# Kernel optimization log

Hardware: AMD Instinct MI355X
Metric: run time of the kernel (lower is better)

Reference implementation:

```python
import jax, jax.numpy as jnp
import numpy as np
from jax import lax
from jax.scipy.special import logsumexp

B, L, D = 64, 256, 512
NUM_CLASS, NREF, NNEG = 10, 50, 100
BLUR = 0.05
EPS_FINAL = BLUR ** 2  # geomloss: eps = blur**p with p=2
MARGIN = 10.0

# epsilon-scaling schedule (geomloss anneals eps geometrically, scaling=0.5),
# then extra iterations at the final eps for convergence.
_sched = []
_e = 8.0
while _e > EPS_FINAL:
    _sched.append(_e)
    _e *= 0.5
_sched += [EPS_FINAL] * 15
EPS_SCHED = jnp.asarray(np.array(_sched, np.float32))


def _cost(x, y):
    # geomloss p=2 cost: |x - y|^2 / 2   -> [N, M]
    return 0.5 * (jnp.sum(x * x, -1)[:, None] + jnp.sum(y * y, -1)[None, :] - 2.0 * (x @ y.T))


def _ot(a, x, b, y):
    """Entropic OT value <a,f>+<b,g> via log-domain Sinkhorn with eps-scaling.
    a,b are (possibly zero-padded) weights; x,y point clouds."""
    C = _cost(x, y)
    loga = jnp.where(a > 0, jnp.log(jnp.maximum(a, 1e-30)), -1e9)
    logb = jnp.where(b > 0, jnp.log(jnp.maximum(b, 1e-30)), -1e9)

    def body(fg, eps):
        f, g = fg
        f = -eps * logsumexp(logb[None, :] + (g[None, :] - C) / eps, axis=1)
        g = -eps * logsumexp(loga[:, None] + (f[:, None] - C) / eps, axis=0)
        return (f, g), None

    (f, g), _ = lax.scan(body, (jnp.zeros_like(a), jnp.zeros_like(b)), EPS_SCHED)
    return jnp.sum(a * f) + jnp.sum(b * g)


def _forward(anchor, weight, anchor_out_neg, t0, grade, grade_neg):
    Cn = t0.shape[0]
    w_ref = jnp.full((t0.shape[1],), 1.0 / t0.shape[1], anchor.dtype)
    w_neg = jnp.full((anchor_out_neg.shape[1],), 1.0 / anchor_out_neg.shape[1], anchor.dtype)

    # cross OT anchor_i vs every class reference cloud: [B, C]
    ot_cross = jax.vmap(lambda a, x: jax.vmap(lambda y: _ot(a, x, w_ref, y))(t0))(weight, anchor)
    # self terms for debiasing
    ot_aa = jax.vmap(lambda a, x: _ot(a, x, a, x))(weight, anchor)            # [B]
    ot_tt = jax.vmap(lambda y: _ot(w_ref, y, w_ref, y))(t0)                    # [C]
    ot_nn = jax.vmap(lambda y: _ot(w_neg, y, w_neg, y))(anchor_out_neg)        # [B]

    # debiased Sinkhorn divergence S = OT_ab - 0.5 OT_aa - 0.5 OT_bb
    S = ot_cross - 0.5 * ot_aa[:, None] - 0.5 * ot_tt[None, :]                 # [B, C]
    pos = jnp.take_along_axis(S, grade[:, None], axis=1)[:, 0]                 # [B]

    # after the torch k-loop, k == num_class-1 (loop-variable leak) -> t0[last]
    t_last = t0[Cn - 1]
    ot_ln = jax.vmap(lambda y: _ot(w_ref, t_last, w_neg, y))(anchor_out_neg)   # [B]
    S_last = ot_ln - 0.5 * ot_tt[Cn - 1] - 0.5 * ot_nn

    t_g = t0[grade_neg]                                                        # [B, NREF, D]
    ot_gn = jax.vmap(lambda yt, yn: _ot(w_ref, yt, w_neg, yn))(t_g, anchor_out_neg)
    S_gn = ot_gn - 0.5 * ot_tt[grade_neg] - 0.5 * ot_nn

    # hinge over all classes k != grade[i], plus the neg-cloud entry (index -1)
    notself = jnp.arange(Cn)[None, :] != grade[:, None]
    hinge_cls = jnp.sum(jnp.where(notself, jax.nn.relu(pos[:, None] - S + MARGIN), 0.0), axis=1)
    hinge_neg = jax.nn.relu(pos - S_last + MARGIN)
    loss_dif = jnp.abs(S_gn - S_last)
    return jnp.mean(hinge_cls + hinge_neg + loss_dif)


def setup_inputs() -> dict:
    key = jax.random.key(0)
    ks = jax.random.split(key, 7)
    anchor = jax.random.normal(ks[0], (B, L, D), jnp.float32)
    length_anchor = jax.random.randint(ks[1], (B,), L // 2, L + 1)
    grade = jax.random.randint(ks[2], (B,), 0, NUM_CLASS)
    w = jax.random.uniform(ks[3], (B, L), jnp.float32, 1e-3, 1.0)
    mask = jnp.arange(L)[None, :] < length_anchor[:, None]
    w = w * mask
    weight = w / jnp.sum(w, axis=1, keepdims=True)  # normalized histogram per sample
    anchor_out_neg = jax.random.normal(ks[4], (B, NNEG, D), jnp.float32)
    grade_neg = jax.random.randint(ks[5], (B,), 0, NUM_CLASS)
    t0 = jax.random.normal(ks[6], (NUM_CLASS, NREF, D), jnp.float32)
    return {"anchor": anchor, "length_anchor": length_anchor, "grade": grade,
            "weight": weight, "anchor_out_neg": anchor_out_neg,
            "grade_neg": grade_neg, "t0": t0, "num_class": NUM_CLASS}


def reference(anchor, length_anchor, grade, weight, anchor_out_neg, grade_neg, t0, num_class):
    # length_anchor is encoded in the zero-padding of `weight` (masked positions
    # have weight 0 and drop out of the OT); num_class == t0.shape[0].
    return _forward(anchor, weight, anchor_out_neg, t0, grade, grade_neg)
```

## Files before the change

kernel.cpp:

```cpp
#include <hip/hip_runtime.h>

#define NB   64
#define LA   256
#define DD   512
#define NCLS 10
#define NREF 50
#define NNEG 100
#define MARGIN 10.0f
#define NITER 27

#define LOG2E 1.44269504f
#define LN2   0.69314718f
#define LC50  (-3.9120230054f)
#define LC100 (-4.6051701860f)

#define OFF_CX   ((size_t)0)
#define SZ_CX    ((size_t)64*500*256)
#define OFF_CAA  (OFF_CX + SZ_CX)
#define SZ_CAA   ((size_t)64*256*256)
#define OFF_CNN  (OFF_CAA + SZ_CAA)
#define SZ_CNN   ((size_t)64*100*100)
#define OFF_CLN  (OFF_CNN + SZ_CNN)
#define SZ_CLN   ((size_t)64*50*100)
#define OFF_CGN  (OFF_CLN + SZ_CLN)
#define SZ_CGN   ((size_t)64*50*100)
#define OFF_CTT  (OFF_CGN + SZ_CGN)
#define SZ_CTT   ((size_t)10*50*50)
#define OFF_SQA  (OFF_CTT + SZ_CTT)
#define OFF_SQN  (OFF_SQA + (size_t)64*256)
#define OFF_SQT  (OFF_SQN + (size_t)64*100)
#define OFF_OTX  (OFF_SQT + (size_t)500)
#define OFF_OTAA (OFF_OTX + (size_t)640)
#define OFF_OTNN (OFF_OTAA + (size_t)64)
#define OFF_OTLN (OFF_OTNN + (size_t)64)
#define OFF_OTGN (OFF_OTLN + (size_t)64)
#define OFF_OTTT (OFF_OTGN + (size_t)64)

__device__ __forceinline__ float eps_at(int it) {
    return (it < 12) ? ldexpf(8.0f, -it) : 0.0025f;
}

__device__ __forceinline__ float block_sum256(float v, float* red, int tid) {
    #pragma unroll
    for (int off = 1; off < 64; off <<= 1) v += __shfl_xor(v, off);
    if ((tid & 63) == 0) red[tid >> 6] = v;
    __syncthreads();
    return red[0] + red[1] + red[2] + red[3];
}

__global__ __launch_bounds__(256) void sq_kernel(const float* __restrict__ anchor,
                                                 const float* __restrict__ neg,
                                                 const float* __restrict__ t0,
                                                 float* __restrict__ ws) {
    int gw   = (blockIdx.x * 256 + threadIdx.x) >> 6;
    int lane = threadIdx.x & 63;
    const int nA = NB * LA, nN = NB * NNEG, nT = NCLS * NREF;
    if (gw >= nA + nN + nT) return;
    const float* row; float* outp;
    if (gw < nA)           { row = anchor + (size_t)gw * DD;          outp = ws + OFF_SQA + gw; }
    else if (gw < nA + nN) { int r = gw - nA;      row = neg + (size_t)r * DD; outp = ws + OFF_SQN + r; }
    else                   { int r = gw - nA - nN; row = t0  + (size_t)r * DD; outp = ws + OFF_SQT + r; }
    const float4* r4 = (const float4*)row;
    float4 u = r4[lane * 2], v = r4[lane * 2 + 1];
    float s = u.x*u.x + u.y*u.y + u.z*u.z + u.w*u.w
            + v.x*v.x + v.y*v.y + v.z*v.z + v.w*v.w;
    #pragma unroll
    for (int off = 1; off < 64; off <<= 1) s += __shfl_xor(s, off);
    if (lane == 0) *outp = 0.5f * s;
}

#define CTM 128
#define CTK 16
__global__ __launch_bounds__(256) void cost128(const float* __restrict__ anchor,
                                               const float* __restrict__ neg,
                                               const float* __restrict__ t0,
                                               const int* __restrict__ gneg,
                                               float* __restrict__ ws) {
    __shared__ __align__(16) float As[CTK][CTM];
    __shared__ __align__(16) float Bs[CTK][CTM];
    int bid = blockIdx.x, tid = threadIdx.x;
    const float *X, *Y, *sqx, *sqy;
    float* Cout; int N, M, ldc, r0, c0;
    bool tr = false;
    if (bid < 512) {
        int b = bid >> 3, t = bid & 7;
        r0 = (t >> 2) * 128; c0 = (t & 3) * 128;
        X = anchor + (size_t)b * LA * DD; Y = t0; N = LA; M = 500; ldc = 500;
        Cout = ws + OFF_CX + (size_t)b * 500 * 256;
        sqx = ws + OFF_SQA + b * LA; sqy = ws + OFF_SQT;
        tr = true;
    } else if (bid < 768) {
        int b2 = bid - 512; int b = b2 >> 2, t = b2 & 3;
        r0 = (t >> 1) * 128; c0 = (t & 1) * 128;
        X = Y = anchor + (size_t)b * LA * DD; N = M = LA; ldc = LA;
        Cout = ws + OFF_CAA + (size_t)b * LA * LA;
        sqx = sqy = ws + OFF_SQA + b * LA;
    } else if (bid < 832) {
        int b = bid - 768; r0 = 0; c0 = 0;
        X = Y = neg + (size_t)b * NNEG * DD; N = M = NNEG; ldc = NNEG;
        Cout = ws + OFF_CNN + (size_t)b * NNEG * NNEG;
        sqx = sqy = ws + OFF_SQN + b * NNEG;
    } else if (bid < 896) {
        int b = bid - 832; r0 = 0; c0 = 0;
        X = t0 + (size_t)9 * NREF * DD; Y = neg + (size_t)b * NNEG * DD;
        N = NREF; M = NNEG; ldc = NNEG;
        Cout = ws + OFF_CLN + (size_t)b * NREF * NNEG;
        sqx = ws + OFF_SQT + 9 * NREF; sqy = ws + OFF_SQN + b * NNEG;
    } else if (bid < 960) {
        int b = bid - 896; r0 = 0; c0 = 0;
        int gc = gneg[b];
        X = t0 + (size_t)gc * NREF * DD; Y = neg + (size_t)b * NNEG * DD;
        N = NREF; M = NNEG; ldc = NNEG;
        Cout = ws + OFF_CGN + (size_t)b * NREF * NNEG;
        sqx = ws + OFF_SQT + gc * NREF; sqy = ws + OFF_SQN + b * NNEG;
    } else {
        int c = bid - 960; r0 = 0; c0 = 0;
        X = Y = t0 + (size_t)c * NREF * DD; N = M = NREF; ldc = NREF;
        Cout = ws + OFF_CTT + (size_t)c * NREF * NREF;
        sqx = sqy = ws + OFF_SQT + c * NREF;
    }
    int row = tid & 127, kq = tid >> 7;
    int tx = tid & 15, ty = tid >> 4;
    bool xok = (r0 + row) < N, yok = (c0 + row) < M;
    const float* xrow = X + (size_t)(r0 + row) * DD + kq * 8;
    const float* yrow = Y + (size_t)(c0 + row) * DD + kq * 8;
    float acc[8][8];
    #pragma unroll
    for (int a = 0; a < 8; a++)
        #pragma unroll
        for (int b = 0; b < 8; b++) acc[a][b] = 0.f;
    for (int k0 = 0; k0 < DD; k0 += CTK) {
        float4 xa0 = xok ? *(const float4*)(xrow + k0)     : make_float4(0,0,0,0);
        float4 xa1 = xok ? *(const float4*)(xrow + k0 + 4) : make_float4(0,0,0,0);
        float4 ya0 = yok ? *(const float4*)(yrow + k0)     : make_float4(0,0,0,0);
        float4 ya1 = yok ? *(const float4*)(yrow + k0 + 4) : make_float4(0,0,0,0);
        __syncthreads();
        int kb = kq * 8;
        As[kb+0][row]=xa0.x; As[kb+1][row]=xa0.y; As[kb+2][row]=xa0.z; As[kb+3][row]=xa0.w;
        As[kb+4][row]=xa1.x; As[kb+5][row]=xa1.y; As[kb+6][row]=xa1.z; As[kb+7][row]=xa1.w;
        Bs[kb+0][row]=ya0.x; Bs[kb+1][row]=ya0.y; Bs[kb+2][row]=ya0.z; Bs[kb+3][row]=ya0.w;
        Bs[kb+4][row]=ya1.x; Bs[kb+5][row]=ya1.y; Bs[kb+6][row]=ya1.z; Bs[kb+7][row]=ya1.w;
        __syncthreads();
        #pragma unroll
        for (int k = 0; k < CTK; k++) {
            float4 a0 = *(const float4*)&As[k][ty << 3];
            float4 a1 = *(const float4*)&As[k][(ty << 3) + 4];
            float4 b0 = *(const float4*)&Bs[k][tx << 3];
            float4 b1 = *(const float4*)&Bs[k][(tx << 3) + 4];
            float av[8] = {a0.x,a0.y,a0.z,a0.w,a1.x,a1.y,a1.z,a1.w};
            float bv[8] = {b0.x,b0.y,b0.z,b0.w,b1.x,b1.y,b1.z,b1.w};
            #pragma unroll
            for (int a = 0; a < 8; a++)
                #pragma unroll
                for (int b = 0; b < 8; b++)
                    acc[a][b] = fmaf(av[a], bv[b], acc[a][b]);
        }
    }
    #pragma unroll
    for (int a = 0; a < 8; a++) {
        int n = r0 + (ty << 3) + a;
        if (n < N) {
            float sx = sqx[n];
            #pragma unroll
            for (int b = 0; b < 8; b++) {
                int m = c0 + (tx << 3) + b;
                if (m < M) {
                    float v = sx + sqy[m] - acc[a][b];
                    if (tr) Cout[(size_t)m * 256 + n] = v;
                    else    Cout[(size_t)n * ldc + m] = v;
                }
            }
        }
    }
}

__global__ __launch_bounds__(1024, 1) void aa_sink_reg(const float* __restrict__ weight,
                                                       float* __restrict__ ws) {
    __shared__ __align__(16) float ahS[256];
    __shared__ float pm[4][256];
    __shared__ float ps[4][256];
    __shared__ float red[16];
    int i = blockIdx.x, tid = threadIdx.x;
    int w = tid >> 6, lane = tid & 63;
    int q = w >> 2;
    int c = ((w & 3) << 6) | lane;
    const float* Cg = ws + OFF_CAA + ((size_t)i << 16);
    float Creg[64];
    #pragma unroll
    for (int k = 0; k < 64; ++k)
        Creg[k] = Cg[(size_t)((q << 6) + k) * 256 + c];
    float wgt = weight[(size_t)i * LA + c];
    float la = (wgt > 0.f) ? __logf(fmaxf(wgt, 1e-30f)) : -1e9f;
    float h = 0.f, fs = 0.f;
    if (q == 0) ahS[c] = 8.0f * la;
    __syncthreads();
    int r4 = q << 4;
    const float4* ah4 = (const float4*)ahS;
    for (int app = 0; app < 54; ++app) {
        float eps = eps_at(app >> 1);
        float m0 = -3.4e38f, m1 = -3.4e38f, m2 = -3.4e38f, m3 = -3.4e38f;
        #pragma unroll
        for (int k = 0; k < 16; ++k) {
            float4 av = ah4[r4 + k];
            m0 = fmaxf(m0, av.x - Creg[4*k+0]);
            m1 = fmaxf(m1, av.y - Creg[4*k+1]);
            m2 = fmaxf(m2, av.z - Creg[4*k+2]);
            m3 = fmaxf(m3, av.w - Creg[4*k+3]);
        }
        pm[q][c] = fmaxf(fmaxf(m0, m1), fmaxf(m2, m3));
        __syncthreads();
        float m = fmaxf(fmaxf(pm[0][c], pm[1][c]), fmaxf(pm[2][c], pm[3][c]));
        float ie2 = (1.0f / eps) * LOG2E;
        float s0 = 0.f, s1 = 0.f, s2 = 0.f, s3 = 0.f;
        #pragma unroll
        for (int k = 0; k < 16; ++k) {
            float4 av = ah4[r4 + k];
            s0 += exp2f((av.x - Creg[4*k+0] - m) * ie2);
            s1 += exp2f((av.y - Creg[4*k+1] - m) * ie2);
            s2 += exp2f((av.z - Creg[4*k+2] - m) * ie2);
            s3 += exp2f((av.w - Creg[4*k+3] - m) * ie2);
        }
        ps[q][c] = (s0 + s1) + (s2 + s3);
        __syncthreads();
        float s = (ps[0][c] + ps[1][c]) + (ps[2][c] + ps[3][c]);
        h = -fmaf(eps * LN2, __log2f(s), m);
        if (app == 52) fs = h;
        if (q == 0) {
            float epsn = eps_at((app + 1) >> 1);
            ahS[c] = fmaf(epsn, la, h);
        }
        __syncthreads();
    }
    float contrib = (q == 0) ? wgt * (fs + h) : 0.f;
    #pragma unroll
    for (int off = 1; off < 64; off <<= 1) contrib += __shfl_xor(contrib, off);
    if (lane == 0) red[w] = contrib;
    __syncthreads();
    if (tid == 0) {
        float s = 0.f;
        #pragma unroll
        for (int k = 0; k < 16; ++k) s += red[k];
        ws[OFF_OTAA + i] = s;
    }
}

__global__ __launch_bounds__(256, 3) void sink_rest(const float* __restrict__ weight,
                                                    float* __restrict__ ws) {
    __shared__ __align__(16) float smem[13324];
    float* red = smem + 13320;
    int bid = blockIdx.x, tid = threadIdx.x;

    if (bid < 640) {
        int ii = bid;
        int i = ii / 10, c = ii - i * 10;
        float* CsT = smem;
        float* agS = smem + 13000;
        float* gSp = smem + 13260;
        const float* Cgbase = ws + OFF_CX + (size_t)i * (500 * 256) + (size_t)c * (50 * 256);
        for (int e = tid; e < 3200; e += 256) {
            int r = e >> 6, n4 = (e & 63) << 2;
            *(float4*)&CsT[r * 260 + n4] = *(const float4*)&Cgbase[(size_t)e << 2];
        }
        float w = weight[(size_t)i * LA + tid];
        float la_r = (w > 0.f) ? __logf(fmaxf(w, 1e-30f)) : -1e9f;
        if (tid < 52) gSp[tid] = (tid < 50) ? 0.f : -1.0e30f;
        __syncthreads();
        float Creg[52];
        #pragma unroll
        for (int r = 0; r < 52; ++r) Creg[r] = (r < 50) ? CsT[r * 260 + tid] : 3.0e30f;
        int grp = tid >> 4, j = tid & 15;
        for (int it = 0; it < NITER; ++it) {
            float eps = eps_at(it), ie2 = (1.0f / eps) * LOG2E;
            {
                const float4* g4 = (const float4*)gSp;
                float m0=-3.4e38f, m1=-3.4e38f, m2=-3.4e38f, m3=-3.4e38f;
                #pragma unroll
                for (int k = 0; k < 13; ++k) {
                    float4 gv = g4[k];
                    m0 = fmaxf(m0, gv.x - Creg[4*k+0]);
                    m1 = fmaxf(m1, gv.y - Creg[4*k+1]);
                    m2 = fmaxf(m2, gv.z - Creg[4*k+2]);
                    m3 = fmaxf(m3, gv.w - Creg[4*k+3]);
                }
                float m = fmaxf(fmaxf(m0, m1), fmaxf(m2, m3));
                float s0=0.f, s1=0.f, s2=0.f, s3=0.f;
                #pragma unroll
                for (int k = 0; k < 13; ++k) {
                    float4 gv = g4[k];
                    s0 += exp2f((gv.x - Creg[4*k+0] - m) * ie2);
                    s1 += exp2f((gv.y - Creg[4*k+1] - m) * ie2);
                    s2 += exp2f((gv.z - Creg[4*k+2] - m) * ie2);
                    s3 += exp2f((gv.w - Creg[4*k+3] - m) * ie2);
                }
                float L = fmaf(eps * LN2, __log2f((s0+s1)+(s2+s3)), m);
                float f = -fmaf(eps, LC50, L);
                agS[tid] = fmaf(eps, la_r, f);
            }
            __syncthreads();
            float4 agr[4];
            #pragma unroll
            for (int q = 0; q < 4; ++q)
                agr[q] = *(const float4*)&agS[(j << 2) + (q << 6)];
            for (int o = grp; o < 50; o += 16) {
                const float* Cr = &CsT[o * 260];
                float u[16];
                #pragma unroll
                for (int q = 0; q < 4; ++q) {
                    float4 cv = *(const float4*)&Cr[(j << 2) + (q << 6)];
                    u[4*q+0] = agr[q].x - cv.x;
                    u[4*q+1] = agr[q].y - cv.y;
                    u[4*q+2] = agr[q].z - cv.z;
                    u[4*q+3] = agr[q].w - cv.w;
                }
                float a0 = fmaxf(fmaxf(u[0], u[4]),  fmaxf(u[8],  u[12]));
                float a1 = fmaxf(fmaxf(u[1], u[5]),  fmaxf(u[9],  u[13]));
                float a2 = fmaxf(fmaxf(u[2], u[6]),  fmaxf(u[10], u[14]));
                float a3 = fmaxf(fmaxf(u[3], u[7]),  fmaxf(u[11], u[15]));
                float m = fmaxf(fmaxf(a0, a1), fmaxf(a2, a3));
                #pragma unroll
                for (int off = 1; off < 16; off <<= 1) m = fmaxf(m, __shfl_xor(m, off));
                float s0=0.f, s1=0.f, s2=0.f, s3=0.f;
                #pragma unroll
                for (int k = 0; k < 16; ++k) {
                    float e = exp2f((u[k] - m) * ie2);
                    if ((k & 3) == 0) s0 += e;
                    else if ((k & 3) == 1) s1 += e;
                    else if ((k & 3) == 2) s2 += e;
                    else s3 += e;
                }
                float s = (s0 + s1) + (s2 + s3);
                #pragma unroll
                for (int off = 1; off < 16; off <<= 1) s += __shfl_xor(s, off);
                if (j == 0) gSp[o] = -fmaf(eps * LN2, __log2f(s), m);
            }
            __syncthreads();
        }
        float f_t = agS[tid] - 0.0025f * la_r;
        float contrib = w * f_t + (tid < 50 ? 0.02f * gSp[tid] : 0.f);
        contrib = block_sum256(contrib, red, tid);
        if (tid == 0) ws[OFF_OTX + ii] = contrib;

    } else if (bid < 704) {
        int inst = bid - 640;
        const float* Cg = ws + OFF_CNN + (size_t)inst * 10000;
        float* ahS = smem;
        float* pmS = smem + 104;
        float* psS = smem + 304;
        bool act = tid < 200;
        int q = tid / 100, c = tid - 100 * q;
        float Creg[52];
        if (act) {
            #pragma unroll
            for (int k = 0; k < 52; ++k) {
                int r = q * 52 + k;
                Creg[k] = (r < 100) ? Cg[(size_t)r * 100 + c] : 3.0e30f;
            }
        }
        if (tid < 100) ahS[tid] = 8.0f * LC100;
        if (tid >= 100 && tid < 104) ahS[tid] = -1.0e30f;
        __syncthreads();
        float h = 0.f, fs = 0.f, m = 0.f;
        for (int app = 0; app < 54; ++app) {
            float eps = eps_at(app >> 1);
            if (act) {
                const float4* ah4 = (const float4*)(ahS + q * 52);
                float m0=-3.4e38f, m1=-3.4e38f, m2=-3.4e38f, m3=-3.4e38f;
                #pragma unroll
                for (int k = 0; k < 13; ++k) {
                    float4 av = ah4[k];
                    m0 = fmaxf(m0, av.x - Creg[4*k+0]);
                    m1 = fmaxf(m1, av.y - Creg[4*k+1]);
                    m2 = fmaxf(m2, av.z - Creg[4*k+2]);
                    m3 = fmaxf(m3, av.w - Creg[4*k+3]);
                }
                pmS[q * 100 + c] = fmaxf(fmaxf(m0, m1), fmaxf(m2, m3));
            }
            __syncthreads();
            if (act) {
                m = fmaxf(pmS[c], pmS[100 + c]);
                float ie2 = (1.0f / eps) * LOG2E;
                const float4* ah4 = (const float4*)(ahS + q * 52);
                float s0=0.f, s1=0.f, s2=0.f, s3=0.f;
                #pragma unroll
                for (int k = 0; k < 13; ++k) {
                    float4 av = ah4[k];
                    s0 += exp2f((av.x - Creg[4*k+0] - m) * ie2);
                    s1 += exp2f((av.y - Creg[4*k+1] - m) * ie2);
                    s2 += exp2f((av.z - Creg[4*k+2] - m) * ie2);
                    s3 += exp2f((av.w - Creg[4*k+3] - m) * ie2);
                }
                psS[q * 100 + c] = (s0 + s1) + (s2 + s3);
            }
            __syncthreads();
            if (act) {
                float s = psS[c] + psS[100 + c];
                h = -fmaf(eps * LN2, __log2f(s), m);
                if (app == 52) fs = h;
                if (q == 0) {
                    float epsn = eps_at((app + 1) >> 1);
                    ahS[c] = fmaf(epsn, LC100, h);
                }
            }
            __syncthreads();
        }
        float contrib = (act && q == 0) ? 0.01f * (fs + h) : 0.f;
        contrib = block_sum256(contrib, red, tid);
        if (tid == 0) ws[OFF_OTNN + inst] = contrib;

    } else if (bid < 832) {
        int q2 = bid - 704;
        const float* Cg = (q2 < 64) ? ws + OFF_CLN + (size_t)q2 * 5000
                                    : ws + OFF_CGN + (size_t)(q2 - 64) * 5000;
        float* outp = (q2 < 64) ? ws + OFF_OTLN + q2 : ws + OFF_OTGN + (q2 - 64);
        float* gSp = smem;
        float* fSp = smem + 100;
        float* pmf = smem + 156;
        float* psf = smem + 406;
        float* pmg = smem + 656;
        float* psg = smem + 856;
        bool actf = tid < 250; int rf = tid / 5, c5 = tid - 5 * rf;
        bool actg = tid < 200; int cg = tid >> 1, hg = tid & 1;
        float Cf[20], Cgr[28];
        if (actf) {
            #pragma unroll
            for (int k = 0; k < 20; ++k) Cf[k] = Cg[(size_t)rf * 100 + c5 * 20 + k];
        }
        if (actg) {
            #pragma unroll
            for (int k = 0; k < 28; ++k) {
                int r = hg * 28 + k;
                Cgr[k] = (r < 50) ? Cg[(size_t)r * 100 + cg] : 3.0e30f;
            }
        }
        if (tid < 100) gSp[tid] = 8.0f * LC100;
        if (tid < 6) fSp[50 + tid] = -1.0e30f;
        __syncthreads();
        float fr = 0.f, gr = 0.f, mf = 0.f, mg = 0.f;
        for (int it = 0; it < NITER; ++it) {
            float eps = eps_at(it), ie2 = (1.0f / eps) * LOG2E;
            if (actf) {
                const float4* g4 = (const float4*)(gSp + c5 * 20);
                float m0=-3.4e38f, m1=-3.4e38f, m2=-3.4e38f, m3=-3.4e38f;
                #pragma unroll
                for (int k = 0; k < 5; ++k) {
                    float4 gv = g4[k];
                    m0 = fmaxf(m0, gv.x - Cf[4*k+0]);
                    m1 = fmaxf(m1, gv.y - Cf[4*k+1]);
                    m2 = fmaxf(m2, gv.z - Cf[4*k+2]);
                    m3 = fmaxf(m3, gv.w - Cf[4*k+3]);
                }
                pmf[c5 * 50 + rf] = fmaxf(fmaxf(m0, m1), fmaxf(m2, m3));
            }
            __syncthreads();
            if (actf) {
                mf = fmaxf(fmaxf(pmf[rf], pmf[50 + rf]),
                     fmaxf(fmaxf(pmf[100 + rf], pmf[150 + rf]), pmf[200 + rf]));
                const float4* g4 = (const float4*)(gSp + c5 * 20);
                float s0=0.f, s1=0.f, s2=0.f, s3=0.f;
                #pragma unroll
                for (int k = 0; k < 5; ++k) {
                    float4 gv = g4[k];
                    s0 += exp2f((gv.x - Cf[4*k+0] - mf) * ie2);
                    s1 += exp2f((gv.y - Cf[4*k+1] - mf) * ie2);
                    s2 += exp2f((gv.z - Cf[4*k+2] - mf) * ie2);
                    s3 += exp2f((gv.w - Cf[4*k+3] - mf) * ie2);
                }
                psf[c5 * 50 + rf] = (s0 + s1) + (s2 + s3);
            }
            __syncthreads();
            if (actf) {
                float s = psf[rf] + psf[50 + rf] + psf[100 + rf] + psf[150 + rf] + psf[200 + rf];
                fr = -fmaf(eps * LN2, __log2f(s), mf);
                if (c5 == 0) fSp[rf] = fmaf(eps, LC50, fr);
            }
            __syncthreads();
            if (actg) {
                const float4* f4 = (const float4*)(fSp + hg * 28);
                float m0=-3.4e38f, m1=-3.4e38f, m2=-3.4e38f, m3=-3.4e38f;
                #pragma unroll
                for (int k = 0; k < 7; ++k) {
                    float4 fv = f4[k];
                    m0 = fmaxf(m0, fv.x - Cgr[4*k+0]);
                    m1 = fmaxf(m1, fv.y - Cgr[4*k+1]);
                    m2 = fmaxf(m2, fv.z - Cgr[4*k+2]);
                    m3 = fmaxf(m3, fv.w - Cgr[4*k+3]);
                }
                pmg[hg * 100 + cg] = fmaxf(fmaxf(m0, m1), fmaxf(m2, m3));
            }
            __syncthreads();
            if (actg) {
                mg = fmaxf(pmg[cg], pmg[100 + cg]);
                const float4* f4 = (const float4*)(fSp + hg * 28);
                float s0=0.f, s1=0.f, s2=0.f, s3=0.f;
                #pragma unroll
                for (int k = 0; k < 7; ++k) {
                    float4 fv = f4[k];
                    s0 += exp2f((fv.x - Cgr[4*k+0] - mg) * ie2);
                    s1 += exp2f((fv.y - Cgr[4*k+1] - mg) * ie2);
                    s2 += exp2f((fv.z - Cgr[4*k+2] - mg) * ie2);
                    s3 += exp2f((fv.w - Cgr[4*k+3] - mg) * ie2);
                }
                psg[hg * 100 + cg] = (s0 + s1) + (s2 + s3);
            }
            __syncthreads();
            if (actg) {
                float s = psg[cg] + psg[100 + cg];
                gr = -fmaf(eps * LN2, __log2f(s), mg);
                if (hg == 0) {
                    float epsn = eps_at(it + 1);
                    gSp[cg] = fmaf(epsn, LC100, gr);
                }
            }
            __syncthreads();
        }
        float contrib = 0.f;
        if (actf && c5 == 0) contrib += 0.02f * fr;
        if (actg && hg == 0) contrib += 0.01f * gr;
        contrib = block_sum256(contrib, red, tid);
        if (tid == 0) *outp = contrib;

    } else {
        int inst = bid - 832;
        const float* Cg = ws + OFF_CTT + (size_t)inst * 2500;
        float* ahS = smem;
        bool act = tid < 50;
        float Creg[52];
        if (act) {
            #pragma unroll
            for (int k = 0; k < 52; ++k)
                Creg[k] = (k < 50) ? Cg[(size_t)k * 50 + tid] : 3.0e30f;
        }
        if (tid < 50) ahS[tid] = 8.0f * LC50;
        if (tid >= 50 && tid < 52) ahS[tid] = -1.0e30f;
        __syncthreads();
        float h = 0.f, fs = 0.f;
        const float4* ah4 = (const float4*)ahS;
        for (int app = 0; app < 54; ++app) {
            float eps = eps_at(app >> 1);
            if (act) {
                float m0=-3.4e38f, m1=-3.4e38f, m2=-3.4e38f, m3=-3.4e38f;
                #pragma unroll
                for (int k = 0; k < 13; ++k) {
                    float4 av = ah4[k];
                    m0 = fmaxf(m0, av.x - Creg[4*k+0]);
                    m1 = fmaxf(m1, av.y - Creg[4*k+1]);
                    m2 = fmaxf(m2, av.z - Creg[4*k+2]);
                    m3 = fmaxf(m3, av.w - Creg[4*k+3]);
                }
                float m = fmaxf(fmaxf(m0, m1), fmaxf(m2, m3));
                float ie2 = (1.0f / eps) * LOG2E;
                float s0=0.f, s1=0.f, s2=0.f, s3=0.f;
                #pragma unroll
                for (int k = 0; k < 13; ++k) {
                    float4 av = ah4[k];
                    s0 += exp2f((av.x - Creg[4*k+0] - m) * ie2);
                    s1 += exp2f((av.y - Creg[4*k+1] - m) * ie2);
                    s2 += exp2f((av.z - Creg[4*k+2] - m) * ie2);
                    s3 += exp2f((av.w - Creg[4*k+3] - m) * ie2);
                }
                h = -fmaf(eps * LN2, __log2f((s0+s1)+(s2+s3)), m);
                if (app == 52) fs = h;
            }
            __syncthreads();
            if (act) {
                float epsn = eps_at((app + 1) >> 1);
                ahS[tid] = fmaf(epsn, LC50, h);
            }
            __syncthreads();
        }
        float contrib = act ? 0.02f * (fs + h) : 0.f;
        contrib = block_sum256(contrib, red, tid);
        if (tid == 0) ws[OFF_OTTT + inst] = contrib;
    }
}

__global__ void assemble_kernel(const int* __restrict__ grade, const int* __restrict__ gneg,
                                const float* __restrict__ ws, float* __restrict__ out) {
    int i = threadIdx.x;
    float total = 0.f;
    if (i < 64) {
        float aa  = ws[OFF_OTAA + i];
        float nn  = ws[OFF_OTNN + i];
        float lnv = ws[OFF_OTLN + i];
        float gnv = ws[OFF_OTGN + i];
        int g  = grade[i];
        int gi = gneg[i];
        float tt9 = ws[OFF_OTTT + 9];
        float ttg = ws[OFF_OTTT + gi];
        float Slast = lnv - 0.5f * tt9 - 0.5f * nn;
        float Sgn   = gnv - 0.5f * ttg - 0.5f * nn;
        float Sv[10];
        #pragma unroll
        for (int k = 0; k < 10; k++)
            Sv[k] = ws[OFF_OTX + i * 10 + k] - 0.5f * aa - 0.5f * ws[OFF_OTTT + k];
        float pos = 0.f;
        #pragma unroll
        for (int k = 0; k < 10; k++) pos = (k == g) ? Sv[k] : pos;
        float hc = 0.f;
        #pragma unroll
        for (int k = 0; k < 10; k++)
            if (k != g) hc += fmaxf(pos - Sv[k] + MARGIN, 0.f);
        float hn = fmaxf(pos - Slast + MARGIN, 0.f);
        total = hc + hn + fabsf(Sgn - Slast);
    }
    #pragma unroll
    for (int off = 1; off < 64; off <<= 1) total += __shfl_xor(total, off);
    if (i == 0) out[0] = total * (1.0f / 64.0f);
}

extern "C" void kernel_launch(void* const* d_in, const int* in_sizes, int n_in,
                              void* d_out, int out_size, void* d_ws, size_t ws_size,
                              hipStream_t stream) {
    const float* anchor = (const float*)d_in[0];
    const int*   grade  = (const int*)d_in[2];
    const float* weight = (const float*)d_in[3];
    const float* neg    = (const float*)d_in[4];
    const int*   gneg   = (const int*)d_in[5];
    const float* t0     = (const float*)d_in[6];
    float* ws  = (float*)d_ws;
    float* out = (float*)d_out;

    sq_kernel      <<<5821, 256, 0, stream>>>(anchor, neg, t0, ws);
    cost128        <<<970, 256, 0, stream>>>(anchor, neg, t0, gneg, ws);
    aa_sink_reg    <<<64, 1024, 0, stream>>>(weight, ws);
    sink_rest      <<<842, 256, 0, stream>>>(weight, ws);
    assemble_kernel<<<1, 64, 0, stream>>>(grade, gneg, ws, out);
}
```

Before: 733.2 us.

## Cut barriers in Sinkhorn loops via shuffles and double-buffered potentials

The aa kernel now places the four row-groups of each column inside one wavefront and combines their partial max and sum with cross-lane shuffles instead of shared-memory partials. Potential vectors are double-buffered, so each iteration needs one barrier instead of three. The nn, ln/gn and tt paths of sink_rest likewise stop splitting rows across threads: each active thread keeps a full row or column of C in registers, which also removes the intermediate barriers. This trades parallelism and higher register use (up to 100 floats per thread) in the small blocks for less synchronisation; the ln/gn path also keeps leftover redundant fr computations.

```diff
diff --git a/kernel.cpp b/kernel.cpp
--- a/kernel.cpp
+++ b/kernel.cpp
@@ -176,62 +176,57 @@
 
 __global__ __launch_bounds__(1024, 1) void aa_sink_reg(const float* __restrict__ weight,
                                                        float* __restrict__ ws) {
-    __shared__ __align__(16) float ahS[256];
-    __shared__ float pm[4][256];
-    __shared__ float ps[4][256];
+    __shared__ __align__(16) float ah[2][256];
     __shared__ float red[16];
     int i = blockIdx.x, tid = threadIdx.x;
     int w = tid >> 6, lane = tid & 63;
-    int q = w >> 2;
-    int c = ((w & 3) << 6) | lane;
+    int c = (w << 4) | (lane & 15);
+    int rg = lane >> 4;
     const float* Cg = ws + OFF_CAA + ((size_t)i << 16);
     float Creg[64];
     #pragma unroll
     for (int k = 0; k < 64; ++k)
-        Creg[k] = Cg[(size_t)((q << 6) + k) * 256 + c];
+        Creg[k] = Cg[(size_t)((rg << 6) + k) * 256 + c];
     float wgt = weight[(size_t)i * LA + c];
     float la = (wgt > 0.f) ? __logf(fmaxf(wgt, 1e-30f)) : -1e9f;
     float h = 0.f, fs = 0.f;
-    if (q == 0) ahS[c] = 8.0f * la;
+    if (rg == 0) ah[0][c] = 8.0f * la;
     __syncthreads();
-    int r4 = q << 4;
-    const float4* ah4 = (const float4*)ahS;
     for (int app = 0; app < 54; ++app) {
         float eps = eps_at(app >> 1);
-        float m0 = -3.4e38f, m1 = -3.4e38f, m2 = -3.4e38f, m3 = -3.4e38f;
+        const float4* a4 = (const float4*)(ah[app & 1]) + (rg << 4);
+        float m0=-3.4e38f, m1=-3.4e38f, m2=-3.4e38f, m3=-3.4e38f;
         #pragma unroll
         for (int k = 0; k < 16; ++k) {
-            float4 av = ah4[r4 + k];
+            float4 av = a4[k];
             m0 = fmaxf(m0, av.x - Creg[4*k+0]);
             m1 = fmaxf(m1, av.y - Creg[4*k+1]);
             m2 = fmaxf(m2, av.z - Creg[4*k+2]);
             m3 = fmaxf(m3, av.w - Creg[4*k+3]);
         }
-        pm[q][c] = fmaxf(fmaxf(m0, m1), fmaxf(m2, m3));
-        __syncthreads();
-        float m = fmaxf(fmaxf(pm[0][c], pm[1][c]), fmaxf(pm[2][c], pm[3][c]));
+        float m = fmaxf(fmaxf(m0, m1), fmaxf(m2, m3));
+        m = fmaxf(m, __shfl_xor(m, 16));
+        m = fmaxf(m, __shfl_xor(m, 32));
         float ie2 = (1.0f / eps) * LOG2E;
-        float s0 = 0.f, s1 = 0.f, s2 = 0.f, s3 = 0.f;
+        float s0=0.f, s1=0.f, s2=0.f, s3=0.f;
         #pragma unroll
         for (int k = 0; k < 16; ++k) {
-            float4 av = ah4[r4 + k];
+            float4 av = a4[k];
             s0 += exp2f((av.x - Creg[4*k+0] - m) * ie2);
             s1 += exp2f((av.y - Creg[4*k+1] - m) * ie2);
             s2 += exp2f((av.z - Creg[4*k+2] - m) * ie2);
             s3 += exp2f((av.w - Creg[4*k+3] - m) * ie2);
         }
-        ps[q][c] = (s0 + s1) + (s2 + s3);
-        __syncthreads();
-        float s = (ps[0][c] + ps[1][c]) + (ps[2][c] + ps[3][c]);
+        float s = (s0 + s1) + (s2 + s3);
+        s += __shfl_xor(s, 16);
+        s += __shfl_xor(s, 32);
         h = -fmaf(eps * LN2, __log2f(s), m);
         if (app == 52) fs = h;
-        if (q == 0) {
-            float epsn = eps_at((app + 1) >> 1);
-            ahS[c] = fmaf(epsn, la, h);
-        }
-        __syncthreads();
-    }
-    float contrib = (q == 0) ? wgt * (fs + h) : 0.f;
+        float epsn = eps_at((app + 1) >> 1);
+        if (rg == 0) ah[(app + 1) & 1][c] = fmaf(epsn, la, h);
+        __syncthreads();
+    }
+    float contrib = (rg == 0) ? wgt * (fs + h) : 0.f;
     #pragma unroll
     for (int off = 1; off < 64; off <<= 1) contrib += __shfl_xor(contrib, off);
     if (lane == 0) red[w] = contrib;
@@ -343,67 +338,48 @@
     } else if (bid < 704) {
         int inst = bid - 640;
         const float* Cg = ws + OFF_CNN + (size_t)inst * 10000;
-        float* ahS = smem;
-        float* pmS = smem + 104;
-        float* psS = smem + 304;
-        bool act = tid < 200;
-        int q = tid / 100, c = tid - 100 * q;
-        float Creg[52];
+        float* ahb = smem;
+        bool act = tid < 100;
+        float Creg[100];
         if (act) {
             #pragma unroll
-            for (int k = 0; k < 52; ++k) {
-                int r = q * 52 + k;
-                Creg[k] = (r < 100) ? Cg[(size_t)r * 100 + c] : 3.0e30f;
-            }
-        }
-        if (tid < 100) ahS[tid] = 8.0f * LC100;
-        if (tid >= 100 && tid < 104) ahS[tid] = -1.0e30f;
-        __syncthreads();
-        float h = 0.f, fs = 0.f, m = 0.f;
+            for (int k = 0; k < 100; ++k) Creg[k] = Cg[(size_t)k * 100 + tid];
+        }
+        if (tid < 100) ahb[tid] = 8.0f * LC100;
+        __syncthreads();
+        float h = 0.f, fs = 0.f;
         for (int app = 0; app < 54; ++app) {
             float eps = eps_at(app >> 1);
             if (act) {
-                const float4* ah4 = (const float4*)(ahS + q * 52);
+                const float4* a4 = (const float4*)(ahb + (app & 1) * 100);
                 float m0=-3.4e38f, m1=-3.4e38f, m2=-3.4e38f, m3=-3.4e38f;
                 #pragma unroll
-                for (int k = 0; k < 13; ++k) {
-                    float4 av = ah4[k];
+                for (int k = 0; k < 25; ++k) {
+                    float4 av = a4[k];
                     m0 = fmaxf(m0, av.x - Creg[4*k+0]);
                     m1 = fmaxf(m1, av.y - Creg[4*k+1]);
                     m2 = fmaxf(m2, av.z - Creg[4*k+2]);
                     m3 = fmaxf(m3, av.w - Creg[4*k+3]);
                 }
-                pmS[q * 100 + c] = fmaxf(fmaxf(m0, m1), fmaxf(m2, m3));
-            }
-            __syncthreads();
-            if (act) {
-                m = fmaxf(pmS[c], pmS[100 + c]);
+                float m = fmaxf(fmaxf(m0, m1), fmaxf(m2, m3));
                 float ie2 = (1.0f / eps) * LOG2E;
-                const float4* ah4 = (const float4*)(ahS + q * 52);
                 float s0=0.f, s1=0.f, s2=0.f, s3=0.f;
                 #pragma unroll
-                for (int k = 0; k < 13; ++k) {
-                    float4 av = ah4[k];
+                for (int k = 0; k < 25; ++k) {
+                    float4 av = a4[k];
                     s0 += exp2f((av.x - Creg[4*k+0] - m) * ie2);
                     s1 += exp2f((av.y - Creg[4*k+1] - m) * ie2);
                     s2 += exp2f((av.z - Creg[4*k+2] - m) * ie2);
                     s3 += exp2f((av.w - Creg[4*k+3] - m) * ie2);
                 }
-                psS[q * 100 + c] = (s0 + s1) + (s2 + s3);
+                h = -fmaf(eps * LN2, __log2f((s0+s1)+(s2+s3)), m);
+                if (app == 52) fs = h;
+                float epsn = eps_at((app + 1) >> 1);
+                ahb[((app + 1) & 1) * 100 + tid] = fmaf(epsn, LC100, h);
             }
             __syncthreads();
-            if (act) {
-                float s = psS[c] + psS[100 + c];
-                h = -fmaf(eps * LN2, __log2f(s), m);
-                if (app == 52) fs = h;
-                if (q == 0) {
-                    float epsn = eps_at((app + 1) >> 1);
-                    ahS[c] = fmaf(epsn, LC100, h);
-                }
-            }
-            __syncthreads();
-        }
-        float contrib = (act && q == 0) ? 0.01f * (fs + h) : 0.f;
+        }
+        float contrib = act ? 0.01f * (fs + h) : 0.f;
         contrib = block_sum256(contrib, red, tid);
         if (tid == 0) ws[OFF_OTNN + inst] = contrib;
 
@@ -412,117 +388,92 @@
         const float* Cg = (q2 < 64) ? ws + OFF_CLN + (size_t)q2 * 5000
                                     : ws + OFF_CGN + (size_t)(q2 - 64) * 5000;
         float* outp = (q2 < 64) ? ws + OFF_OTLN + q2 : ws + OFF_OTGN + (q2 - 64);
-        float* gSp = smem;
-        float* fSp = smem + 100;
-        float* pmf = smem + 156;
-        float* psf = smem + 406;
-        float* pmg = smem + 656;
-        float* psg = smem + 856;
-        bool actf = tid < 250; int rf = tid / 5, c5 = tid - 5 * rf;
-        bool actg = tid < 200; int cg = tid >> 1, hg = tid & 1;
-        float Cf[20], Cgr[28];
+        float* gS = smem;
+        float* fS = smem + 104;
+        bool actf = tid < 50;
+        bool actg = (tid >= 64) && (tid < 164);
+        int cg = tid - 64;
+        float Creg[100];
         if (actf) {
             #pragma unroll
-            for (int k = 0; k < 20; ++k) Cf[k] = Cg[(size_t)rf * 100 + c5 * 20 + k];
-        }
-        if (actg) {
-            #pragma unroll
-            for (int k = 0; k < 28; ++k) {
-                int r = hg * 28 + k;
-                Cgr[k] = (r < 50) ? Cg[(size_t)r * 100 + cg] : 3.0e30f;
-            }
-        }
-        if (tid < 100) gSp[tid] = 8.0f * LC100;
-        if (tid < 6) fSp[50 + tid] = -1.0e30f;
-        __syncthreads();
-        float fr = 0.f, gr = 0.f, mf = 0.f, mg = 0.f;
+            for (int k = 0; k < 100; ++k) Creg[k] = Cg[(size_t)tid * 100 + k];
+        } else if (actg) {
+            #pragma unroll
+            for (int k = 0; k < 52; ++k)
+                Creg[k] = (k < 50) ? Cg[(size_t)k * 100 + cg] : 3.0e30f;
+        }
+        if (tid < 100) gS[tid] = 8.0f * LC100;
+        if (tid == 0) { fS[50] = -1.0e30f; fS[51] = -1.0e30f; }
+        __syncthreads();
+        float fr = 0.f, gr = 0.f;
         for (int it = 0; it < NITER; ++it) {
             float eps = eps_at(it), ie2 = (1.0f / eps) * LOG2E;
             if (actf) {
-                const float4* g4 = (const float4*)(gSp + c5 * 20);
+                const float4* g4 = (const float4*)gS;
                 float m0=-3.4e38f, m1=-3.4e38f, m2=-3.4e38f, m3=-3.4e38f;
                 #pragma unroll
-                for (int k = 0; k < 5; ++k) {
+                for (int k = 0; k < 25; ++k) {
                     float4 gv = g4[k];
-                    m0 = fmaxf(m0, gv.x - Cf[4*k+0]);
-                    m1 = fmaxf(m1, gv.y - Cf[4*k+1]);
-                    m2 = fmaxf(m2, gv.z - Cf[4*k+2]);
-                    m3 = fmaxf(m3, gv.w - Cf[4*k+3]);
-                }
-                pmf[c5 * 50 + rf] = fmaxf(fmaxf(m0, m1), fmaxf(m2, m3));
-            }
-            __syncthreads();
-            if (actf) {
-                mf = fmaxf(fmaxf(pmf[rf], pmf[50 + rf]),
-                     fmaxf(fmaxf(pmf[100 + rf], pmf[150 + rf]), pmf[200 + rf]));
-                const float4* g4 = (const float4*)(gSp + c5 * 20);
+                    m0 = fmaxf(m0, gv.x - Creg[4*k+0]);
+                    m1 = fmaxf(m1, gv.y - Creg[4*k+1]);
+                    m2 = fmaxf(m2, gv.z - Creg[4*k+2]);
+                    m3 = fmaxf(m3, gv.w - Creg[4*k+3]);
+                }
+                float m = fmaxf(fmaxf(m0, m1), fmaxf(m2, m3));
                 float s0=0.f, s1=0.f, s2=0.f, s3=0.f;
                 #pragma unroll
-                for (int k = 0; k < 5; ++k) {
+                for (int k = 0; k < 25; ++k) {
                     float4 gv = g4[k];
-                    s0 += exp2f((gv.x - Cf[4*k+0] - mf) * ie2);
-                    s1 += exp2f((gv.y - Cf[4*k+1] - mf) * ie2);
-                    s2 += exp2f((gv.z - Cf[4*k+2] - mf) * ie2);
-                    s3 += exp2f((gv.w - Cf[4*k+3] - mf) * ie2);
-                }
-                psf[c5 * 50 + rf] = (s0 + s1) + (s2 + s3);
-            }
-            __syncthreads();
-            if (actf) {
-                float s = psf[rf] + psf[50 + rf] + psf[100 + rf] + psf[150 + rf] + psf[200 + rf];
-                fr = -fmaf(eps * LN2, __log2f(s), mf);
-                if (c5 == 0) fSp[rf] = fmaf(eps, LC50, fr);
+                    s0 += exp2f((gv.x - Creg[4*k+0] - m) * ie2);
+                    s1 += exp2f((gv.y - Creg[4*k+1] - m) * ie2);
+                    s2 += exp2f((gv.z - Creg[4*k+2] - m) * ie2);
+                    s3 += exp2f((gv.w - Creg[4*k+3] - m) * ie2);
+                }
+                fr = -fmaf(eps * LN2, __log2f((s0+s1)+(s2+s3)),
+                           fmaf(eps, LC100, m) - fmaf(eps, LC100, m) + m);
+                fr = -fmaf(eps * LN2, __log2f((s0+s1)+(s2+s3)), m);
+                fr = fr - eps * LC100;
+                fr = -fmaf(eps * LN2, __log2f((s0+s1)+(s2+s3)), m);
+                fS[tid] = fmaf(eps, LC50, fr);
             }
             __syncthreads();
             if (actg) {
-                const float4* f4 = (const float4*)(fSp + hg * 28);
+                const float4* f4 = (const float4*)fS;
                 float m0=-3.4e38f, m1=-3.4e38f, m2=-3.4e38f, m3=-3.4e38f;
                 #pragma unroll
-                for (int k = 0; k < 7; ++k) {
+                for (int k = 0; k < 13; ++k) {
                     float4 fv = f4[k];
-                    m0 = fmaxf(m0, fv.x - Cgr[4*k+0]);
-                    m1 = fmaxf(m1, fv.y - Cgr[4*k+1]);
-                    m2 = fmaxf(m2, fv.z - Cgr[4*k+2]);
-                    m3 = fmaxf(m3, fv.w - Cgr[4*k+3]);
-                }
-                pmg[hg * 100 + cg] = fmaxf(fmaxf(m0, m1), fmaxf(m2, m3));
+                    m0 = fmaxf(m0, fv.x - Creg[4*k+0]);
+                    m1 = fmaxf(m1, fv.y - Creg[4*k+1]);
+                    m2 = fmaxf(m2, fv.z - Creg[4*k+2]);
+                    m3 = fmaxf(m3, fv.w - Creg[4*k+3]);
+                }
+                float m = fmaxf(fmaxf(m0, m1), fmaxf(m2, m3));
+                float s0=0.f, s1=0.f, s2=0.f, s3=0.f;
+                #pragma unroll
+                for (int k = 0; k < 13; ++k) {
+                    float4 fv = f4[k];
+                    s0 += exp2f((fv.x - Creg[4*k+0] - m) * ie2);
+                    s1 += exp2f((fv.y - Creg[4*k+1] - m) * ie2);
+                    s2 += exp2f((fv.z - Creg[4*k+2] - m) * ie2);
+                    s3 += exp2f((fv.w - Creg[4*k+3] - m) * ie2);
+                }
+                gr = -fmaf(eps * LN2, __log2f((s0+s1)+(s2+s3)), m);
+                float epsn = eps_at(it + 1);
+                gS[cg] = fmaf(epsn, LC100, gr);
             }
             __syncthreads();
-            if (actg) {
-                mg = fmaxf(pmg[cg], pmg[100 + cg]);
-                const float4* f4 = (const float4*)(fSp + hg * 28);
-                float s0=0.f, s1=0.f, s2=0.f, s3=0.f;
-                #pragma unroll
-                for (int k = 0; k < 7; ++k) {
-                    float4 fv = f4[k];
-                    s0 += exp2f((fv.x - Cgr[4*k+0] - mg) * ie2);
-                    s1 += exp2f((fv.y - Cgr[4*k+1] - mg) * ie2);
-                    s2 += exp2f((fv.z - Cgr[4*k+2] - mg) * ie2);
-                    s3 += exp2f((fv.w - Cgr[4*k+3] - mg) * ie2);
-                }
-                psg[hg * 100 + cg] = (s0 + s1) + (s2 + s3);
-            }
-            __syncthreads();
-            if (actg) {
-                float s = psg[cg] + psg[100 + cg];
-                gr = -fmaf(eps * LN2, __log2f(s), mg);
-                if (hg == 0) {
-                    float epsn = eps_at(it + 1);
-                    gSp[cg] = fmaf(epsn, LC100, gr);
-                }
-            }
-            __syncthreads();
         }
         float contrib = 0.f;
-        if (actf && c5 == 0) contrib += 0.02f * fr;
-        if (actg && hg == 0) contrib += 0.01f * gr;
+        if (actf) contrib += 0.02f * fr;
+        if (actg) contrib += 0.01f * gr;
         contrib = block_sum256(contrib, red, tid);
         if (tid == 0) *outp = contrib;
 
     } else {
         int inst = bid - 832;
         const float* Cg = ws + OFF_CTT + (size_t)inst * 2500;
-        float* ahS = smem;
+        float* ahb = smem;
         bool act = tid < 50;
         float Creg[52];
         if (act) {
@@ -530,18 +481,18 @@
             for (int k = 0; k < 52; ++k)
                 Creg[k] = (k < 50) ? Cg[(size_t)k * 50 + tid] : 3.0e30f;
         }
-        if (tid < 50) ahS[tid] = 8.0f * LC50;
-        if (tid >= 50 && tid < 52) ahS[tid] = -1.0e30f;
+        if (tid < 50) ahb[tid] = 8.0f * LC50;
+        if (tid >= 50 && tid < 52) { ahb[tid] = -1.0e30f; ahb[52 + tid] = -1.0e30f; }
         __syncthreads();
         float h = 0.f, fs = 0.f;
-        const float4* ah4 = (const float4*)ahS;
         for (int app = 0; app < 54; ++app) {
             float eps = eps_at(app >> 1);
             if (act) {
+                const float4* a4 = (const float4*)(ahb + (app & 1) * 52);
                 float m0=-3.4e38f, m1=-3.4e38f, m2=-3.4e38f, m3=-3.4e38f;
                 #pragma unroll
                 for (int k = 0; k < 13; ++k) {
-                    float4 av = ah4[k];
+                    float4 av = a4[k];
                     m0 = fmaxf(m0, av.x - Creg[4*k+0]);
                     m1 = fmaxf(m1, av.y - Creg[4*k+1]);
                     m2 = fmaxf(m2, av.z - Creg[4*k+2]);
@@ -552,7 +503,7 @@
                 float s0=0.f, s1=0.f, s2=0.f, s3=0.f;
                 #pragma unroll
                 for (int k = 0; k < 13; ++k) {
-                    float4 av = ah4[k];
+                    float4 av = a4[k];
                     s0 += exp2f((av.x - Creg[4*k+0] - m) * ie2);
                     s1 += exp2f((av.y - Creg[4*k+1] - m) * ie2);
                     s2 += exp2f((av.z - Creg[4*k+2] - m) * ie2);
@@ -560,11 +511,8 @@
                 }
                 h = -fmaf(eps * LN2, __log2f((s0+s1)+(s2+s3)), m);
                 if (app == 52) fs = h;
-            }
-            __syncthreads();
-            if (act) {
                 float epsn = eps_at((app + 1) >> 1);
-                ahS[tid] = fmaf(epsn, LC50, h);
+                ahb[((app + 1) & 1) * 52 + tid] = fmaf(epsn, LC50, h);
             }
             __syncthreads();
         }
```

Result: slower. 887.2 us (+21.0%).
